# Performance work log

Measured on AMD Instinct MI355X. Metric: run time of the kernel, lower is better.

## Reference

```python
import jax, jax.numpy as jnp
import numpy as np

DEPTH = 7  # complete binary trees with 2**DEPTH = 128 leaves

B, L = 4096, 128
V, E, OUT = 100000, 128, 3


def setup_inputs() -> dict:
    key = jax.random.key(0)
    ks = jax.random.split(key, 6)
    tokens = jax.random.randint(ks[0], (B, L), 0, V, dtype=jnp.int64)
    embedding = jax.random.normal(ks[1], (V, E), dtype=jnp.float32)
    # tree_layer: Linear(2E -> E); torch stores weight as [out, in]
    W_tree = jax.random.normal(ks[2], (E, 2 * E), dtype=jnp.float32) * (1.0 / np.sqrt(2 * E))
    b_tree = jax.random.normal(ks[3], (E,), dtype=jnp.float32) * 0.01
    # classifier_layer: Linear(E -> OUT)
    W_cls = jax.random.normal(ks[4], (OUT, E), dtype=jnp.float32) * (1.0 / np.sqrt(E))
    b_cls = jax.random.normal(ks[5], (OUT,), dtype=jnp.float32) * 0.01
    return {"tokens": tokens, "embedding": embedding, "W_tree": W_tree,
            "b_tree": b_tree, "W_cls": W_cls, "b_cls": b_cls}


def reference(tokens, embedding, W_tree, b_tree, W_cls, b_cls):
    # Leaf embeddings: gather rows of the embedding table. [B, L, E]
    reps = embedding[tokens]
    # Level-synchronous bottom-up composition (depth-batched across all trees):
    # at each level, pair adjacent nodes, concat features, apply tree_layer + tanh.
    for _ in range(DEPTH):
        left = reps[:, 0::2, :]   # [B, n/2, E]
        right = reps[:, 1::2, :]  # [B, n/2, E]
        combined = jnp.concatenate([left, right], axis=-1)  # [B, n/2, 2E]
        reps = jnp.tanh(jnp.einsum('bnh,eh->bne', combined, W_tree) + b_tree)
    roots = reps[:, 0, :]  # [B, E]
    return roots @ W_cls.T + b_cls  # [B, OUT]
```

## Files before the change

kernel.cpp:

```cpp
#include <hip/hip_runtime.h>
#include <hip/hip_fp16.h>


typedef _Float16 half8 __attribute__((ext_vector_type(8)));
typedef float floatx4 __attribute__((ext_vector_type(4)));

#define STRIDE 264
#define UROW   33
#define NPAIR  2048

__device__ __forceinline__ float fast_tanh(float x) {
  float e = __expf(2.f * x);
  return 1.f - 2.f * __builtin_amdgcn_rcpf(e + 1.f);
}

__device__ __forceinline__ unsigned pkrtz(float a, float b) {
  auto h = __builtin_amdgcn_cvt_pkrtz(a, b);
  return __builtin_bit_cast(unsigned, h);
}

__device__ __forceinline__ void gather_leafhalf(int tok, const float* __restrict__ emb,
                                                _Float16* buf, int row, int seg) {
  const float4* src = (const float4*)emb + (size_t)tok * 32 + (seg & 1) * 16;
  uint4* dst = (uint4*)buf + row * UROW + seg * 8;
#pragma unroll
  for (int j = 0; j < 8; ++j) {
    float4 x = src[2 * j], y = src[2 * j + 1];
    uint4 w;
    w.x = pkrtz(x.x, x.y); w.y = pkrtz(x.z, x.w);
    w.z = pkrtz(y.x, y.y); w.w = pkrtz(y.z, y.w);
    dst[j] = w;
  }
}

__device__ __forceinline__ void mfma_k256(const _Float16* arow, const half8 (&Wf)[2][8],
                                          floatx4 (&accO)[2]) {
  floatx4 aA[2], aB[2];
  aA[0] = (floatx4){0.f, 0.f, 0.f, 0.f}; aA[1] = (floatx4){0.f, 0.f, 0.f, 0.f};
  aB[0] = (floatx4){0.f, 0.f, 0.f, 0.f}; aB[1] = (floatx4){0.f, 0.f, 0.f, 0.f};
#pragma unroll
  for (int ks = 0; ks < 4; ++ks) {
    half8 x0 = *(const half8*)(arow + ks * 32);
    half8 x1 = *(const half8*)(arow + (ks + 4) * 32);
    aA[0] = __builtin_amdgcn_mfma_f32_16x16x32_f16(x0, Wf[0][ks],     aA[0], 0, 0, 0);
    aB[0] = __builtin_amdgcn_mfma_f32_16x16x32_f16(x1, Wf[0][ks + 4], aB[0], 0, 0, 0);
    aA[1] = __builtin_amdgcn_mfma_f32_16x16x32_f16(x0, Wf[1][ks],     aA[1], 0, 0, 0);
    aB[1] = __builtin_amdgcn_mfma_f32_16x16x32_f16(x1, Wf[1][ks + 4], aB[1], 0, 0, 0);
  }
  accO[0] = aA[0] + aB[0];
  accO[1] = aA[1] + aB[1];
}

template<int MT, int MOUT, int RCLAMP>
__device__ __forceinline__ void level_std(
    const _Float16* inb, _Float16* outb,
    const half8 (&Wf)[2][8], const float (&bias)[2],
    int nbase, int l15, int quad)
{
  floatx4 acc[MT][2];
  if (MT == 1) {
    const int rr = (RCLAMP < 15) ? (l15 < RCLAMP ? l15 : RCLAMP) : l15;
    floatx4 a2[2];
    mfma_k256(inb + rr * STRIDE + quad * 8, Wf, a2);
    acc[0][0] = a2[0]; acc[0][1] = a2[1];
  } else {
#pragma unroll
    for (int m = 0; m < MT; ++m) {
      acc[m][0] = (floatx4){0.f, 0.f, 0.f, 0.f};
      acc[m][1] = (floatx4){0.f, 0.f, 0.f, 0.f};
    }
#pragma unroll
    for (int m = 0; m < MT; ++m) {
      const _Float16* arow = inb + (m * 16 + l15) * STRIDE + quad * 8;
#pragma unroll
      for (int ks = 0; ks < 8; ++ks) {
        half8 a = *(const half8*)(arow + ks * 32);
        acc[m][0] = __builtin_amdgcn_mfma_f32_16x16x32_f16(a, Wf[0][ks], acc[m][0], 0, 0, 0);
        acc[m][1] = __builtin_amdgcn_mfma_f32_16x16x32_f16(a, Wf[1][ks], acc[m][1], 0, 0, 0);
      }
    }
  }

  const int mrow = quad * 4;
#pragma unroll
  for (int m = 0; m < MT; ++m)
#pragma unroll
    for (int i = 0; i < 2; ++i) {
      const int col = (nbase + i) * 16 + l15;
#pragma unroll
      for (int r = 0; r < 4; ++r) {
        const int node = m * 16 + mrow + r;
        if (node < MOUT) {
          float v = fast_tanh(acc[m][i][r] + bias[i]);
          outb[(node >> 1) * STRIDE + (node & 1) * 128 + col] = (_Float16)v;
        }
      }
    }
}

__global__ __launch_bounds__(256, 3)
void tree_kernel(const int* __restrict__ tokens,
                 const float* __restrict__ embedding,
                 const float* __restrict__ W_tree,
                 const float* __restrict__ b_tree,
                 const float* __restrict__ W_cls,
                 const float* __restrict__ b_cls,
                 float* __restrict__ out)
{
  __shared__ __align__(16) _Float16 bufA[64 * STRIDE];
  __shared__ __align__(16) _Float16 bufB[32 * STRIDE];
  __shared__ __align__(16) _Float16 bufC[4 * STRIDE];
  __shared__ float wavepart[4][2][3];

  const int tid  = threadIdx.x;
  const int wid  = tid >> 6;
  const int lane = tid & 63;
  const int l15  = lane & 15;
  const int quad = lane >> 4;
  const int nbase = wid * 2;
  const int row  = tid & 63;
  const int seg  = tid >> 6;
  const int tidx = 2 * row + (seg >> 1);

  half8 Wf[2][8];
#pragma unroll
  for (int i = 0; i < 2; ++i) {
    const int e = (nbase + i) * 16 + l15;
#pragma unroll
    for (int ks = 0; ks < 8; ++ks) {
      const int k = ks * 32 + quad * 8;
      const float4* p = (const float4*)(W_tree + e * 256 + k);
      float4 lo = p[0], hi = p[1];
      half8 f;
      f[0] = (_Float16)lo.x; f[1] = (_Float16)lo.y; f[2] = (_Float16)lo.z; f[3] = (_Float16)lo.w;
      f[4] = (_Float16)hi.x; f[5] = (_Float16)hi.y; f[6] = (_Float16)hi.z; f[7] = (_Float16)hi.w;
      Wf[i][ks] = f;
    }
  }
  float bias[2];
#pragma unroll
  for (int i = 0; i < 2; ++i) bias[i] = b_tree[(nbase + i) * 16 + l15];

  float wc[2][3];
#pragma unroll
  for (int i = 0; i < 2; ++i) {
    const int col = (nbase + i) * 16 + l15;
#pragma unroll
    for (int o = 0; o < 3; ++o) wc[i][o] = W_cls[o * 128 + col];
  }

  int tokA = tokens[(2 * blockIdx.x) * 128 + tidx];

#pragma unroll 1
  for (int p = blockIdx.x; p < NPAIR; p += gridDim.x) {
    int pn = p + gridDim.x;
    if (pn >= NPAIR) pn = p;

    gather_leafhalf(tokA, embedding, bufA, row, seg);
    const int tokB = tokens[(2 * p + 1) * 128 + tidx];
    __syncthreads();

    level_std<4, 64, 15>(bufA, bufB, Wf, bias, nbase, l15, quad);
    __syncthreads();
    level_std<2, 32, 15>(bufB, bufA, Wf, bias, nbase, l15, quad);
    __syncthreads();
    level_std<1, 16, 15>(bufA, bufB, Wf, bias, nbase, l15, quad);
    __syncthreads();
    level_std<1,  8,  7>(bufB, bufA, Wf, bias, nbase, l15, quad);
    __syncthreads();
    level_std<1,  4,  3>(bufA, bufC, Wf, bias, nbase, l15, quad);
    __syncthreads();

    gather_leafhalf(tokB, embedding, bufA, row, seg);
    tokA = tokens[(2 * pn) * 128 + tidx];
    __syncthreads();

    level_std<4, 64, 15>(bufA, bufB, Wf, bias, nbase, l15, quad);
    __syncthreads();
    level_std<2, 32, 15>(bufB, bufA, Wf, bias, nbase, l15, quad);
    __syncthreads();
    level_std<1, 16, 15>(bufA, bufB, Wf, bias, nbase, l15, quad);
    __syncthreads();
    level_std<1,  8,  7>(bufB, bufA, Wf, bias, nbase, l15, quad);
    __syncthreads();
    level_std<1,  4,  3>(bufA, bufC + 2 * STRIDE, Wf, bias, nbase, l15, quad);
    __syncthreads();

    {
      const int rclamp = l15 < 4 ? l15 : 3;
      floatx4 acc[2];
      mfma_k256(bufC + rclamp * STRIDE + quad * 8, Wf, acc);
      const int mrow = quad * 4;
#pragma unroll
      for (int i = 0; i < 2; ++i) {
        const int col = (nbase + i) * 16 + l15;
#pragma unroll
        for (int r = 0; r < 4; ++r) {
          const int mr = mrow + r;
          if (mr < 4) {
            float v = fast_tanh(acc[i][r] + bias[i]);
            bufA[(mr >> 1) * STRIDE + (mr & 1) * 128 + col] = (_Float16)v;
          }
        }
      }
    }
    __syncthreads();

    {
      const int rclamp = l15 < 2 ? l15 : 1;
      floatx4 acc[2];
      mfma_k256(bufA + rclamp * STRIDE + quad * 8, Wf, acc);
      float part[2][3] = {{0.f, 0.f, 0.f}, {0.f, 0.f, 0.f}};
      if (quad == 0) {
#pragma unroll
        for (int i = 0; i < 2; ++i) {
#pragma unroll
          for (int rr = 0; rr < 2; ++rr) {
            float v = fast_tanh(acc[i][rr] + bias[i]);
#pragma unroll
            for (int o = 0; o < 3; ++o) part[rr][o] = fmaf(v, wc[i][o], part[rr][o]);
          }
        }
      }
#pragma unroll
      for (int rr = 0; rr < 2; ++rr) {
#pragma unroll
        for (int o = 0; o < 3; ++o) {
          float v = part[rr][o];
          v += __shfl_down(v, 8);
          v += __shfl_down(v, 4);
          v += __shfl_down(v, 2);
          v += __shfl_down(v, 1);
          if (lane == 0) wavepart[wid][rr][o] = v;
        }
      }
    }
    __syncthreads();
    if (tid < 6) {
      const int rr = tid / 3, o = tid - 3 * rr;
      float v = wavepart[0][rr][o] + wavepart[1][rr][o]
              + wavepart[2][rr][o] + wavepart[3][rr][o];
      out[(2 * p + rr) * 3 + o] = v + b_cls[o];
    }
  }
}

extern "C" void kernel_launch(void* const* d_in, const int* in_sizes, int n_in,
                              void* d_out, int out_size, void* d_ws, size_t ws_size,
                              hipStream_t stream) {
  const int*   tokens    = (const int*)d_in[0];
  const float* embedding = (const float*)d_in[1];
  const float* W_tree    = (const float*)d_in[2];
  const float* b_tree    = (const float*)d_in[3];
  const float* W_cls     = (const float*)d_in[4];
  const float* b_cls     = (const float*)d_in[5];
  float* out = (float*)d_out;

  dim3 grid(768), block(256);
  tree_kernel<<<grid, block, 0, stream>>>(tokens, embedding, W_tree, b_tree, W_cls, b_cls, out);
}
```

Measured before the change: 156.1 us.

## Overlap next tree's embedding gather with small late tree levels

Moves the leaf embedding gather for the next tree so it runs in two halves alongside the low-parallelism levels (8 and 4 nodes) of the current tree. Those levels now ping-pong within bufB, which leaves bufA free to receive the gather. The aim is to hide global gather latency behind the short MFMA levels and remove the dedicated barrier-separated gather phases. In exchange, register pressure and instruction mixing rise during those levels, and the buffer reuse between levels has to stay correct.

Result: slower. 167.0 us (+7.0%).

```diff
diff --git a/kernel.cpp b/kernel.cpp
--- a/kernel.cpp
+++ b/kernel.cpp
@@ -19,12 +19,13 @@
   return __builtin_bit_cast(unsigned, h);
 }
 
-__device__ __forceinline__ void gather_leafhalf(int tok, const float* __restrict__ emb,
-                                                _Float16* buf, int row, int seg) {
+template<int J0, int J1>
+__device__ __forceinline__ void gather_chunk(int tok, const float* __restrict__ emb,
+                                             _Float16* buf, int row, int seg) {
   const float4* src = (const float4*)emb + (size_t)tok * 32 + (seg & 1) * 16;
   uint4* dst = (uint4*)buf + row * UROW + seg * 8;
 #pragma unroll
-  for (int j = 0; j < 8; ++j) {
+  for (int j = J0; j < J1; ++j) {
     float4 x = src[2 * j], y = src[2 * j + 1];
     uint4 w;
     w.x = pkrtz(x.x, x.y); w.y = pkrtz(x.z, x.w);
@@ -149,41 +150,43 @@
     for (int o = 0; o < 3; ++o) wc[i][o] = W_cls[o * 128 + col];
   }
 
-  int tokA = tokens[(2 * blockIdx.x) * 128 + tidx];
+  {
+    const int tok = tokens[(2 * blockIdx.x) * 128 + tidx];
+    gather_chunk<0, 8>(tok, embedding, bufA, row, seg);
+  }
+  __syncthreads();
 
 #pragma unroll 1
   for (int p = blockIdx.x; p < NPAIR; p += gridDim.x) {
     int pn = p + gridDim.x;
     if (pn >= NPAIR) pn = p;
 
-    gather_leafhalf(tokA, embedding, bufA, row, seg);
+    level_std<4, 64, 15>(bufA, bufB, Wf, bias, nbase, l15, quad);
     const int tokB = tokens[(2 * p + 1) * 128 + tidx];
     __syncthreads();
+    level_std<2, 32, 15>(bufB, bufA, Wf, bias, nbase, l15, quad);
+    __syncthreads();
+    level_std<1, 16, 15>(bufA, bufB, Wf, bias, nbase, l15, quad);
+    __syncthreads();
+    gather_chunk<0, 4>(tokB, embedding, bufA, row, seg);
+    level_std<1, 8, 7>(bufB, bufB + 8 * STRIDE, Wf, bias, nbase, l15, quad);
+    __syncthreads();
+    gather_chunk<4, 8>(tokB, embedding, bufA, row, seg);
+    level_std<1, 4, 3>(bufB + 8 * STRIDE, bufC, Wf, bias, nbase, l15, quad);
+    __syncthreads();
 
     level_std<4, 64, 15>(bufA, bufB, Wf, bias, nbase, l15, quad);
+    const int tokA2 = tokens[(2 * pn) * 128 + tidx];
     __syncthreads();
     level_std<2, 32, 15>(bufB, bufA, Wf, bias, nbase, l15, quad);
     __syncthreads();
     level_std<1, 16, 15>(bufA, bufB, Wf, bias, nbase, l15, quad);
     __syncthreads();
-    level_std<1,  8,  7>(bufB, bufA, Wf, bias, nbase, l15, quad);
-    __syncthreads();
-    level_std<1,  4,  3>(bufA, bufC, Wf, bias, nbase, l15, quad);
-    __syncthreads();
-
-    gather_leafhalf(tokB, embedding, bufA, row, seg);
-    tokA = tokens[(2 * pn) * 128 + tidx];
-    __syncthreads();
-
-    level_std<4, 64, 15>(bufA, bufB, Wf, bias, nbase, l15, quad);
-    __syncthreads();
-    level_std<2, 32, 15>(bufB, bufA, Wf, bias, nbase, l15, quad);
-    __syncthreads();
-    level_std<1, 16, 15>(bufA, bufB, Wf, bias, nbase, l15, quad);
-    __syncthreads();
-    level_std<1,  8,  7>(bufB, bufA, Wf, bias, nbase, l15, quad);
-    __syncthreads();
-    level_std<1,  4,  3>(bufA, bufC + 2 * STRIDE, Wf, bias, nbase, l15, quad);
+    gather_chunk<0, 4>(tokA2, embedding, bufA, row, seg);
+    level_std<1, 8, 7>(bufB, bufB + 8 * STRIDE, Wf, bias, nbase, l15, quad);
+    __syncthreads();
+    gather_chunk<4, 8>(tokA2, embedding, bufA, row, seg);
+    level_std<1, 4, 3>(bufB + 8 * STRIDE, bufC + 2 * STRIDE, Wf, bias, nbase, l15, quad);
     __syncthreads();
 
     {
@@ -199,7 +202,7 @@
           const int mr = mrow + r;
           if (mr < 4) {
             float v = fast_tanh(acc[i][r] + bias[i]);
-            bufA[(mr >> 1) * STRIDE + (mr & 1) * 128 + col] = (_Float16)v;
+            bufB[(mr >> 1) * STRIDE + (mr & 1) * 128 + col] = (_Float16)v;
           }
         }
       }
@@ -209,7 +212,7 @@
     {
       const int rclamp = l15 < 2 ? l15 : 1;
       floatx4 acc[2];
-      mfma_k256(bufA + rclamp * STRIDE + quad * 8, Wf, acc);
+      mfma_k256(bufB + rclamp * STRIDE + quad * 8, Wf, acc);
       float part[2][3] = {{0.f, 0.f, 0.f}, {0.f, 0.f, 0.f}};
       if (quad == 0) {
 #pragma unroll
```
